# Kernel tuning notes

Measured on AMD Instinct MI355X. Metric: run time of the kernel, lower is better.

## Reference

```python
import jax, jax.numpy as jnp
import numpy as np

PATCH_SIZE = 9
EPS = 1e-05


def to_patches(x, p):
    # x: [b, c, H, W] -> [b, c*(H-p+1)*(W-p+1), p, p]
    # matches torch unfold(2,p,1).unfold(3,p,1) + rearrange 'b c p1 p2 h w -> b (c p1 p2) h w'
    b, c, H, W = x.shape
    Hp, Wp = H - p + 1, W - p + 1
    # fixed small loop over p*p offsets (p=9); XLA fuses these slices
    pat = jnp.stack([x[:, :, i:i + Hp, j:j + Wp] for i in range(p) for j in range(p)], axis=2)
    pat = pat.reshape(b, c, p, p, Hp, Wp)
    pat = jnp.transpose(pat, (0, 1, 4, 5, 2, 3))  # b c Hp Wp p p
    return pat.reshape(b, c * Hp * Wp, p, p)


def _norm(x, eps):
    # per-channel normalization over last two dims (population variance, correction=0)
    mu = jnp.mean(x, axis=(-1, -2), keepdims=True)
    var = jnp.mean((x - mu) ** 2, axis=(-1, -2), keepdims=True) + eps
    return (x - mu) / jnp.sqrt(var)


def setup_inputs() -> dict:
    key = jax.random.key(0)
    k1, k2, k3 = jax.random.split(key, 3)
    b, c, H, W, p = 8, 1, 128, 128, PATCH_SIZE
    Hp, Wp = H - p + 1, W - p + 1
    x1 = jax.random.normal(k1, (b, c, H, W), dtype=jnp.float32)
    x2 = jax.random.normal(k2, (b, c, H, W), dtype=jnp.float32)
    mask2 = jax.random.uniform(k3, (b, c * Hp * Wp, p, p), dtype=jnp.float32)
    return {"x1": x1, "x2": x2, "mask2": mask2}


def reference(x1, x2, mask2):
    p = PATCH_SIZE
    x1p = to_patches(x1, p)
    x2p = to_patches(x2, p)
    _, c, h, w = x1p.shape
    x2p = x2p * mask2
    x1n = _norm(x1p, EPS)
    x2n = _norm(x2p, EPS)
    score = jnp.einsum('bchw,bchw->b', x1n, x2n)
    return score / (c * h * w)
```

## Files before the change

kernel.cpp:

```cpp
#include <hip/hip_runtime.h>


#define BATCH 8
#define HH    128
#define WW    128
#define PP    9
#define HP    120
#define WP    120
#define NPATCH (HP * WP)
#define PSQ   (PP * PP)
#define EPSF  1e-5f
#define CP    60
#define XW    72
#define NBLK  (BATCH * HP * 2)

__device__ __forceinline__ void gload16(const void* g, void* lds) {
    __builtin_amdgcn_global_load_lds(
        (const __attribute__((address_space(1))) void*)g,
        (__attribute__((address_space(3))) void*)lds, 16, 0, 0);
}

__global__ __launch_bounds__(128) void ncc_kernel(const float* __restrict__ x1,
                                                  const float* __restrict__ x2,
                                                  const float* __restrict__ mask,
                                                  float* __restrict__ part)
{
    const int blk  = blockIdx.x;
    const int b    = blk / 240;
    const int rest = blk - b * 240;
    const int i    = rest >> 1;
    const int j0   = (rest & 1) * CP;
    const int tid  = threadIdx.x;
    const int lane = tid & 63;

    __shared__ __align__(16) float m_lds[CP * PSQ];
    __shared__ __align__(16) float x_lds[2][PP][XW];
    __shared__ float wsum[2];

    {
        const float4* msrc = reinterpret_cast<const float4*>(
            mask + ((size_t)b * NPATCH + (size_t)i * WP + j0) * PSQ);
        char* mdst = reinterpret_cast<char*>(m_lds);
        #pragma unroll
        for (int k = 0; k < 10; ++k) {
            int g = k * 128 + tid;
            if (g < (CP * PSQ) / 4)
                gload16(msrc + g, mdst + (size_t)(g - lane) * 16);
        }
    }
    {
        const float4* s1 = reinterpret_cast<const float4*>(
            x1 + ((size_t)(b * HH + i)) * WW + j0);
        const float4* s2 = reinterpret_cast<const float4*>(
            x2 + ((size_t)(b * HH + i)) * WW + j0);
        char* d1 = reinterpret_cast<char*>(&x_lds[0][0][0]);
        char* d2 = reinterpret_cast<char*>(&x_lds[1][0][0]);
        #pragma unroll
        for (int k = 0; k < 2; ++k) {
            int t = k * 128 + tid;
            if (t < (PP * XW) / 4) {
                int r  = t / (XW / 4);
                int c4 = t - r * (XW / 4);
                gload16(s1 + r * (WW / 4) + c4, d1 + (size_t)(t - lane) * 16);
                gload16(s2 + r * (WW / 4) + c4, d2 + (size_t)(t - lane) * 16);
            }
        }
    }
    __syncthreads();

    float val = 0.0f;
    const int j = tid >> 1;
    const int h = tid & 1;
    if (j < CP) {
        const int r0 = h ? 5 : 0;
        const int r1 = h ? 9 : 5;
        float sa = 0.f, saa = 0.f, sb = 0.f, sbb = 0.f, sab = 0.f;
        const float* mp = m_lds + j * PSQ + h * 45;
        for (int r = r0; r < r1; ++r) {
            const float* x1r = &x_lds[0][r][j];
            const float* x2r = &x_lds[1][r][j];
            #pragma unroll
            for (int cc = 0; cc < PP; ++cc) {
                float a  = x1r[cc];
                float bv = x2r[cc] * mp[cc];
                sa += a;
                saa = fmaf(a, a, saa);
                sb += bv;
                sbb = fmaf(bv, bv, sbb);
                sab = fmaf(a, bv, sab);
            }
            mp += PP;
        }
        sa  += __shfl_xor(sa, 1);
        saa += __shfl_xor(saa, 1);
        sb  += __shfl_xor(sb, 1);
        sbb += __shfl_xor(sbb, 1);
        sab += __shfl_xor(sab, 1);
        if (h == 0) {
            const float invN = 1.0f / 81.0f;
            float mua  = sa * invN;
            float mub  = sb * invN;
            float vara = saa * invN - mua * mua + EPSF;
            float varb = sbb * invN - mub * mub + EPSF;
            float cov  = sab - 81.0f * mua * mub;
            val = cov / sqrtf(vara * varb);
        }
    }

    #pragma unroll
    for (int off = 32; off > 0; off >>= 1)
        val += __shfl_down(val, off);
    if ((tid & 63) == 0) wsum[tid >> 6] = val;
    __syncthreads();
    if (tid == 0)
        part[blk] = wsum[0] + wsum[1];
}

__global__ __launch_bounds__(256) void finalize_kernel(const float* __restrict__ part,
                                                       float* __restrict__ out)
{
    const int b = blockIdx.x;
    const int t = threadIdx.x;
    float v = (t < 240) ? part[b * 240 + t] : 0.0f;
    #pragma unroll
    for (int off = 32; off > 0; off >>= 1)
        v += __shfl_down(v, off);
    __shared__ float s[4];
    if ((t & 63) == 0) s[t >> 6] = v;
    __syncthreads();
    if (t == 0)
        out[b] = (s[0] + s[1] + s[2] + s[3]) * (1.0f / ((float)NPATCH * (float)PSQ));
}

extern "C" void kernel_launch(void* const* d_in, const int* in_sizes, int n_in,
                              void* d_out, int out_size, void* d_ws, size_t ws_size,
                              hipStream_t stream) {
    const float* x1   = (const float*)d_in[0];
    const float* x2   = (const float*)d_in[1];
    const float* mask = (const float*)d_in[2];
    float* out  = (float*)d_out;
    float* part = (float*)d_ws;

    ncc_kernel<<<NBLK, 128, 0, stream>>>(x1, x2, mask, part);
    finalize_kernel<<<BATCH, 256, 0, stream>>>(part, out);
}
```

Measured before the change: 17.56 us.

## Split mask staging into two chunks overlapped with compute, four threads per patch

Each block's mask tile is now staged in two chunks of up to 32 patches. The second chunk is issued after the first barrier so its global-to-LDS transfer can overlap with computing the first chunk. Columns are split at 64 instead of 60, so the two halves process 64 and 56 patches; the second half clamps its x-row reads to stay in bounds. Each patch is now handled by four threads covering two rows each, with the last thread also taking row 8, and partials are combined with two xor shuffles. This raises thread utilisation but leaves the h==3 lanes with more work, and adds a second barrier phase.

After: 19.33 us. 1.1x slower.

```diff
diff --git a/kernel.cpp b/kernel.cpp
--- a/kernel.cpp
+++ b/kernel.cpp
@@ -10,8 +10,6 @@
 #define NPATCH (HP * WP)
 #define PSQ   (PP * PP)
 #define EPSF  1e-5f
-#define CP    60
-#define XW    72
 #define NBLK  (BATCH * HP * 2)
 
 __device__ __forceinline__ void gload16(const void* g, void* lds) {
@@ -29,81 +27,100 @@
     const int b    = blk / 240;
     const int rest = blk - b * 240;
     const int i    = rest >> 1;
-    const int j0   = (rest & 1) * CP;
+    const int half = rest & 1;
+    const int j0   = half << 6;
     const int tid  = threadIdx.x;
     const int lane = tid & 63;
 
-    __shared__ __align__(16) float m_lds[CP * PSQ];
-    __shared__ __align__(16) float x_lds[2][PP][XW];
+    const int RW  = half ? 68 : 72;
+    const int NW4 = half ? 17 : 18;
+
+    __shared__ __align__(16) float m_lds[2][32 * PSQ];
+    __shared__ __align__(16) float x_lds[2][9 * 72];
     __shared__ float wsum[2];
 
     {
-        const float4* msrc = reinterpret_cast<const float4*>(
-            mask + ((size_t)b * NPATCH + (size_t)i * WP + j0) * PSQ);
-        char* mdst = reinterpret_cast<char*>(m_lds);
-        #pragma unroll
-        for (int k = 0; k < 10; ++k) {
-            int g = k * 128 + tid;
-            if (g < (CP * PSQ) / 4)
-                gload16(msrc + g, mdst + (size_t)(g - lane) * 16);
-        }
-    }
-    {
-        const float4* s1 = reinterpret_cast<const float4*>(
-            x1 + ((size_t)(b * HH + i)) * WW + j0);
-        const float4* s2 = reinterpret_cast<const float4*>(
-            x2 + ((size_t)(b * HH + i)) * WW + j0);
-        char* d1 = reinterpret_cast<char*>(&x_lds[0][0][0]);
-        char* d2 = reinterpret_cast<char*>(&x_lds[1][0][0]);
+        char* d1 = (char*)&x_lds[0][0];
+        char* d2 = (char*)&x_lds[1][0];
         #pragma unroll
         for (int k = 0; k < 2; ++k) {
             int t = k * 128 + tid;
-            if (t < (PP * XW) / 4) {
-                int r  = t / (XW / 4);
-                int c4 = t - r * (XW / 4);
-                gload16(s1 + r * (WW / 4) + c4, d1 + (size_t)(t - lane) * 16);
-                gload16(s2 + r * (WW / 4) + c4, d2 + (size_t)(t - lane) * 16);
+            if (t < 9 * NW4) {
+                int r, c4;
+                if (half) { r = t / 17; c4 = t - r * 17; }
+                else      { r = t / 18; c4 = t - r * 18; }
+                int sc4 = (half && c4 > 15) ? 15 : c4;
+                const size_t rowf = ((size_t)(b * HH + i + r)) * WW + j0;
+                gload16(x1 + rowf + sc4 * 4, d1 + (size_t)(t - lane) * 16);
+                gload16(x2 + rowf + sc4 * 4, d2 + (size_t)(t - lane) * 16);
             }
         }
     }
-    __syncthreads();
+
+    auto stage_mask = [&](int cb) {
+        const int cnt4 = ((half && cb) ? 24 : 32) * PSQ / 4;
+        const float4* msrc = (const float4*)(
+            mask + ((size_t)b * NPATCH + (size_t)i * WP + j0 + 32 * cb) * PSQ);
+        char* mdst = (char*)&m_lds[cb][0];
+        #pragma unroll
+        for (int k = 0; k < 6; ++k) {
+            int t = k * 128 + tid;
+            if (t < cnt4)
+                gload16(msrc + t, mdst + (size_t)(t - lane) * 16);
+        }
+    };
+
+    stage_mask(0);
 
     float val = 0.0f;
-    const int j = tid >> 1;
-    const int h = tid & 1;
-    if (j < CP) {
-        const int r0 = h ? 5 : 0;
-        const int r1 = h ? 9 : 5;
-        float sa = 0.f, saa = 0.f, sb = 0.f, sbb = 0.f, sab = 0.f;
-        const float* mp = m_lds + j * PSQ + h * 45;
-        for (int r = r0; r < r1; ++r) {
-            const float* x1r = &x_lds[0][r][j];
-            const float* x2r = &x_lds[1][r][j];
+    #pragma unroll
+    for (int cb = 0; cb < 2; ++cb) {
+        __syncthreads();
+        if (cb == 0) stage_mask(1);
+
+        const int npat = (half && cb) ? 24 : 32;
+        const int pl   = tid >> 2;
+        const int h    = tid & 3;
+        if (pl < npat) {
+            float sa = 0.f, saa = 0.f, sb = 0.f, sbb = 0.f, sab = 0.f;
+            const float* mp = &m_lds[cb][pl * PSQ + 18 * h];
+            const int col = 32 * cb + pl;
+            const float* xa = &x_lds[0][2 * h * RW + col];
+            const float* xb = &x_lds[1][2 * h * RW + col];
             #pragma unroll
-            for (int cc = 0; cc < PP; ++cc) {
-                float a  = x1r[cc];
-                float bv = x2r[cc] * mp[cc];
-                sa += a;
-                saa = fmaf(a, a, saa);
-                sb += bv;
-                sbb = fmaf(bv, bv, sbb);
+            for (int t = 0; t < 18; ++t) {
+                const int tr = t / 9, c = t - 9 * tr;
+                float a  = xa[tr * RW + c];
+                float bv = xb[tr * RW + c] * mp[t];
+                sa += a;  saa = fmaf(a, a, saa);
+                sb += bv; sbb = fmaf(bv, bv, sbb);
                 sab = fmaf(a, bv, sab);
             }
-            mp += PP;
-        }
-        sa  += __shfl_xor(sa, 1);
-        saa += __shfl_xor(saa, 1);
-        sb  += __shfl_xor(sb, 1);
-        sbb += __shfl_xor(sbb, 1);
-        sab += __shfl_xor(sab, 1);
-        if (h == 0) {
-            const float invN = 1.0f / 81.0f;
-            float mua  = sa * invN;
-            float mub  = sb * invN;
-            float vara = saa * invN - mua * mua + EPSF;
-            float varb = sbb * invN - mub * mub + EPSF;
-            float cov  = sab - 81.0f * mua * mub;
-            val = cov / sqrtf(vara * varb);
+            if (h == 3) {
+                #pragma unroll
+                for (int t = 18; t < 27; ++t) {
+                    const int c = t - 18;
+                    float a  = xa[2 * RW + c];
+                    float bv = xb[2 * RW + c] * mp[t];
+                    sa += a;  saa = fmaf(a, a, saa);
+                    sb += bv; sbb = fmaf(bv, bv, sbb);
+                    sab = fmaf(a, bv, sab);
+                }
+            }
+            sa  += __shfl_xor(sa, 1);  sa  += __shfl_xor(sa, 2);
+            saa += __shfl_xor(saa, 1); saa += __shfl_xor(saa, 2);
+            sb  += __shfl_xor(sb, 1);  sb  += __shfl_xor(sb, 2);
+            sbb += __shfl_xor(sbb, 1); sbb += __shfl_xor(sbb, 2);
+            sab += __shfl_xor(sab, 1); sab += __shfl_xor(sab, 2);
+            if (h == 0) {
+                const float invN = 1.0f / 81.0f;
+                float mua  = sa * invN;
+                float mub  = sb * invN;
+                float vara = saa * invN - mua * mua + EPSF;
+                float varb = sbb * invN - mub * mub + EPSF;
+                float cov  = sab - 81.0f * mua * mub;
+                val += cov / sqrtf(vara * varb);
+            }
         }
     }
 
```

## Process two output rows per block with double-buffered mask staging

Applied to the files above, without the earlier changes.

Each block now covers two patch rows (four 60-patch chunks) instead of one half-row. It loads ten input rows once and double-buffers the mask chunks in LDS, so the next chunk's load overlaps compute on the current one. This is meant to cut redundant input-row loads and per-block launch overhead, and the finalize kernel shrinks to a single wavefront. The cost is four times fewer blocks and more LDS per block, which lowers memory-level parallelism on a kernel dominated by streaming the mask.

Measured after the change: 19.16 us. 9.1% more time.

```diff
diff --git a/kernel.cpp b/kernel.cpp
--- a/kernel.cpp
+++ b/kernel.cpp
@@ -10,9 +10,9 @@
 #define NPATCH (HP * WP)
 #define PSQ   (PP * PP)
 #define EPSF  1e-5f
-#define CP    60
-#define XW    72
-#define NBLK  (BATCH * HP * 2)
+#define CHUNKP 60
+#define CHUNKF (CHUNKP * PSQ)
+#define NBLK  (BATCH * HP / 2)
 
 __device__ __forceinline__ void gload16(const void* g, void* lds) {
     __builtin_amdgcn_global_load_lds(
@@ -26,84 +26,88 @@
                                                   float* __restrict__ part)
 {
     const int blk  = blockIdx.x;
-    const int b    = blk / 240;
-    const int rest = blk - b * 240;
-    const int i    = rest >> 1;
-    const int j0   = (rest & 1) * CP;
+    const int b    = blk / 60;
+    const int i0   = (blk - b * 60) * 2;
     const int tid  = threadIdx.x;
     const int lane = tid & 63;
 
-    __shared__ __align__(16) float m_lds[CP * PSQ];
-    __shared__ __align__(16) float x_lds[2][PP][XW];
+    __shared__ __align__(16) float m_lds[2][CHUNKF];
+    __shared__ __align__(16) float x_lds[2][10 * WW];
     __shared__ float wsum[2];
 
     {
-        const float4* msrc = reinterpret_cast<const float4*>(
-            mask + ((size_t)b * NPATCH + (size_t)i * WP + j0) * PSQ);
-        char* mdst = reinterpret_cast<char*>(m_lds);
+        const float4* s1 = (const float4*)(x1 + ((size_t)(b * HH + i0)) * WW);
+        const float4* s2 = (const float4*)(x2 + ((size_t)(b * HH + i0)) * WW);
+        char* d1 = (char*)&x_lds[0][0];
+        char* d2 = (char*)&x_lds[1][0];
         #pragma unroll
-        for (int k = 0; k < 10; ++k) {
-            int g = k * 128 + tid;
-            if (g < (CP * PSQ) / 4)
-                gload16(msrc + g, mdst + (size_t)(g - lane) * 16);
-        }
-    }
-    {
-        const float4* s1 = reinterpret_cast<const float4*>(
-            x1 + ((size_t)(b * HH + i)) * WW + j0);
-        const float4* s2 = reinterpret_cast<const float4*>(
-            x2 + ((size_t)(b * HH + i)) * WW + j0);
-        char* d1 = reinterpret_cast<char*>(&x_lds[0][0][0]);
-        char* d2 = reinterpret_cast<char*>(&x_lds[1][0][0]);
-        #pragma unroll
-        for (int k = 0; k < 2; ++k) {
+        for (int k = 0; k < 3; ++k) {
             int t = k * 128 + tid;
-            if (t < (PP * XW) / 4) {
-                int r  = t / (XW / 4);
-                int c4 = t - r * (XW / 4);
-                gload16(s1 + r * (WW / 4) + c4, d1 + (size_t)(t - lane) * 16);
-                gload16(s2 + r * (WW / 4) + c4, d2 + (size_t)(t - lane) * 16);
+            if (t < 320) {
+                gload16(s1 + t, d1 + (size_t)(t - lane) * 16);
+                gload16(s2 + t, d2 + (size_t)(t - lane) * 16);
             }
         }
     }
-    __syncthreads();
+
+    auto stage_mask = [&](int k) {
+        const int row = i0 + (k >> 1);
+        const int jh  = k & 1;
+        const float4* msrc = (const float4*)(
+            mask + ((size_t)b * NPATCH + (size_t)row * WP + CHUNKP * jh) * PSQ);
+        char* mdst = (char*)&m_lds[k & 1][0];
+        #pragma unroll
+        for (int q = 0; q < 10; ++q) {
+            int t = q * 128 + tid;
+            if (t < CHUNKF / 4)
+                gload16(msrc + t, mdst + (size_t)(t - lane) * 16);
+        }
+    };
+
+    stage_mask(0);
 
     float val = 0.0f;
-    const int j = tid >> 1;
-    const int h = tid & 1;
-    if (j < CP) {
-        const int r0 = h ? 5 : 0;
-        const int r1 = h ? 9 : 5;
-        float sa = 0.f, saa = 0.f, sb = 0.f, sbb = 0.f, sab = 0.f;
-        const float* mp = m_lds + j * PSQ + h * 45;
-        for (int r = r0; r < r1; ++r) {
-            const float* x1r = &x_lds[0][r][j];
-            const float* x2r = &x_lds[1][r][j];
-            #pragma unroll
-            for (int cc = 0; cc < PP; ++cc) {
-                float a  = x1r[cc];
-                float bv = x2r[cc] * mp[cc];
-                sa += a;
-                saa = fmaf(a, a, saa);
-                sb += bv;
-                sbb = fmaf(bv, bv, sbb);
-                sab = fmaf(a, bv, sab);
+    #pragma unroll
+    for (int k = 0; k < 4; ++k) {
+        __syncthreads();
+        if (k < 3) stage_mask(k + 1);
+
+        const int pl = tid >> 1;
+        const int h  = tid & 1;
+        if (pl < CHUNKP) {
+            const int r2 = k >> 1;
+            const int j  = CHUNKP * (k & 1) + pl;
+            const int rr0 = h ? 5 : 0;
+            const int rr1 = h ? 9 : 5;
+            float sa = 0.f, saa = 0.f, sb = 0.f, sbb = 0.f, sab = 0.f;
+            const float* mp = &m_lds[k & 1][pl * PSQ + rr0 * PP];
+            for (int r = rr0; r < rr1; ++r) {
+                const float* x1r = &x_lds[0][(r2 + r) * WW + j];
+                const float* x2r = &x_lds[1][(r2 + r) * WW + j];
+                #pragma unroll
+                for (int cc = 0; cc < PP; ++cc) {
+                    float a  = x1r[cc];
+                    float bv = x2r[cc] * mp[cc];
+                    sa += a;  saa = fmaf(a, a, saa);
+                    sb += bv; sbb = fmaf(bv, bv, sbb);
+                    sab = fmaf(a, bv, sab);
+                }
+                mp += PP;
             }
-            mp += PP;
-        }
-        sa  += __shfl_xor(sa, 1);
-        saa += __shfl_xor(saa, 1);
-        sb  += __shfl_xor(sb, 1);
-        sbb += __shfl_xor(sbb, 1);
-        sab += __shfl_xor(sab, 1);
-        if (h == 0) {
-            const float invN = 1.0f / 81.0f;
-            float mua  = sa * invN;
-            float mub  = sb * invN;
-            float vara = saa * invN - mua * mua + EPSF;
-            float varb = sbb * invN - mub * mub + EPSF;
-            float cov  = sab - 81.0f * mua * mub;
-            val = cov / sqrtf(vara * varb);
+            sa  += __shfl_xor(sa, 1);
+            saa += __shfl_xor(saa, 1);
+            sb  += __shfl_xor(sb, 1);
+            sbb += __shfl_xor(sbb, 1);
+            sab += __shfl_xor(sab, 1);
+            if (h == 0) {
+                const float invN = 1.0f / 81.0f;
+                float mua  = sa * invN;
+                float mub  = sb * invN;
+                float vara = saa * invN - mua * mua + EPSF;
+                float varb = sbb * invN - mub * mub + EPSF;
+                float cov  = sab - 81.0f * mua * mub;
+                val += cov / sqrtf(vara * varb);
+            }
         }
     }
 
@@ -116,20 +120,17 @@
         part[blk] = wsum[0] + wsum[1];
 }
 
-__global__ __launch_bounds__(256) void finalize_kernel(const float* __restrict__ part,
-                                                       float* __restrict__ out)
+__global__ __launch_bounds__(64) void finalize_kernel(const float* __restrict__ part,
+                                                      float* __restrict__ out)
 {
     const int b = blockIdx.x;
     const int t = threadIdx.x;
-    float v = (t < 240) ? part[b * 240 + t] : 0.0f;
+    float v = (t < 60) ? part[b * 60 + t] : 0.0f;
     #pragma unroll
     for (int off = 32; off > 0; off >>= 1)
         v += __shfl_down(v, off);
-    __shared__ float s[4];
-    if ((t & 63) == 0) s[t >> 6] = v;
-    __syncthreads();
     if (t == 0)
-        out[b] = (s[0] + s[1] + s[2] + s[3]) * (1.0f / ((float)NPATCH * (float)PSQ));
+        out[b] = v * (1.0f / ((float)NPATCH * (float)PSQ));
 }
 
 extern "C" void kernel_launch(void* const* d_in, const int* in_sizes, int n_in,
@@ -142,5 +143,5 @@
     float* part = (float*)d_ws;
 
     ncc_kernel<<<NBLK, 128, 0, stream>>>(x1, x2, mask, part);
-    finalize_kernel<<<BATCH, 256, 0, stream>>>(part, out);
+    finalize_kernel<<<BATCH, 64, 0, stream>>>(part, out);
 }
```
